# Kernel tuning notes

Measured on AMD Instinct MI355X. Metric: run time of the kernel, lower is better.

Reference implementation:

```python
import jax, jax.numpy as jnp
import numpy as np

NUM_HEADS = 4

def setup_inputs() -> dict:
    key = jax.random.key(0)
    ks = jax.random.split(key, 5)
    B, N, C = 2, 4096, 256
    s = 0.02
    return {
        "x": jax.random.normal(ks[0], (B, N, C), dtype=jnp.float32),
        "qkv_w": jax.random.normal(ks[1], (3 * C, C), dtype=jnp.float32) * s,
        "qkv_b": jax.random.normal(ks[2], (3 * C,), dtype=jnp.float32) * s,
        "out_w": jax.random.normal(ks[3], (C, C), dtype=jnp.float32) * s,
        "out_b": jax.random.normal(ks[4], (C,), dtype=jnp.float32) * s,
    }

def reference(x, qkv_w, qkv_b, out_w, out_b):
    # x: [B, N, C]; manual multi-head self-attention (eval mode, dropout off)
    B, N, C = x.shape
    H = NUM_HEADS
    D = C // H
    qkv = x @ qkv_w.T + qkv_b                      # [B, N, 3C]
    qkv = qkv.reshape(B, N, 3, H, D)
    qkv = jnp.transpose(qkv, (2, 0, 3, 1, 4))      # [3, B, H, N, D]
    q, k, v = qkv[0], qkv[1], qkv[2]
    scale = D ** -0.5
    attn = jnp.einsum('bhnd,bhmd->bhnm', q, k) * scale  # [B, H, N, N]
    attn = jax.nn.softmax(attn, axis=-1)
    out = jnp.einsum('bhnm,bhmd->bhnd', attn, v)   # [B, H, N, D]
    out = jnp.transpose(out, (0, 2, 1, 3)).reshape(B, N, C)
    return out @ out_w.T + out_b
```

## Files before the change

### kernel.cpp

```cpp
#include <hip/hip_runtime.h>

typedef __bf16 bf16x8 __attribute__((ext_vector_type(8)));
typedef float f32x4 __attribute__((ext_vector_type(4)));

#define MFMA_BF16(a, b, c) __builtin_amdgcn_mfma_f32_16x16x32_bf16((a), (b), (c), 0, 0, 0)

#define C1 0.18033688f

static __device__ __forceinline__ unsigned short f2bf(float f) {
    unsigned int u = __float_as_uint(f);
    unsigned int r = (u + 0x7fffu + ((u >> 16) & 1u)) >> 16;
    return (unsigned short)r;
}
static __device__ __forceinline__ float bf2f(unsigned short us) {
    return __uint_as_float(((unsigned int)us) << 16);
}
static __device__ __forceinline__ float exp2_hw(float x) {
    float r;
    asm("v_exp_f32 %0, %1" : "=v"(r) : "v"(x));
    return r;
}
static __device__ __forceinline__ unsigned pack_rh(float a, float b) {
    return __byte_perm(__float_as_uint(a) + 0x8000u, __float_as_uint(b) + 0x8000u, 0x7632);
}
static __device__ __forceinline__ void gload16(const void* g, void* l) {
    __builtin_amdgcn_global_load_lds(
        (const __attribute__((address_space(1))) unsigned int*)g,
        (__attribute__((address_space(3))) unsigned int*)l, 16, 0, 0);
}

static __device__ __forceinline__ void conv_seg8(const void* src, unsigned short* dst, int n,
                                                 int lb, bool f32) {
    const int base = lb * 2048 + (int)threadIdx.x * 8;
    if (base < n) {
        if (f32) {
            const float4 u0 = *(const float4*)((const float*)src + base);
            const float4 u1 = *(const float4*)((const float*)src + base + 4);
            uint4 p;
            p.x = pack_rh(u0.x, u0.y);
            p.y = pack_rh(u0.z, u0.w);
            p.z = pack_rh(u1.x, u1.y);
            p.w = pack_rh(u1.z, u1.w);
            *(uint4*)(dst + base) = p;
        } else {
            *(uint4*)(dst + base) = *(const uint4*)((const unsigned short*)src + base);
        }
    }
}

__global__ __launch_bounds__(256) void convert_kernel(
    const void* __restrict__ x, const void* __restrict__ qw, const void* __restrict__ qb,
    const void* __restrict__ ow, const void* __restrict__ ob,
    unsigned short* __restrict__ xb, unsigned short* __restrict__ qwb,
    unsigned short* __restrict__ qbb, unsigned short* __restrict__ owb,
    unsigned short* __restrict__ obb, int* __restrict__ flag) {
    __shared__ int tot;
    if (threadIdx.x == 0) tot = 0;
    __syncthreads();
    {
        unsigned short v = ((const unsigned short*)x)[threadIdx.x];
        int e = (v >> 7) & 0xFF;
        if (e >= 195) atomicAdd(&tot, 1);
    }
    __syncthreads();
    const bool f32 = (tot >= 8);
    if (blockIdx.x == 0 && threadIdx.x == 0) flag[0] = f32 ? 1 : 0;

    const int bid = blockIdx.x;
    if (bid < 1024)       conv_seg8(x,  xb,  2097152, bid,        f32);
    else if (bid < 1120)  conv_seg8(qw, qwb, 196608,  bid - 1024, f32);
    else if (bid < 1121)  conv_seg8(qb, qbb, 768,     bid - 1120, f32);
    else if (bid < 1153)  conv_seg8(ow, owb, 65536,   bid - 1121, f32);
    else                  conv_seg8(ob, obb, 256,     bid - 1153, f32);
}

template <bool QKV>
__global__ __launch_bounds__(256) void gemm_kernel(
    const unsigned short* __restrict__ A, const unsigned short* __restrict__ W,
    const unsigned short* __restrict__ bias, unsigned short* __restrict__ Cb,
    float* __restrict__ Cf, const int* __restrict__ flag,
    unsigned short* __restrict__ Vt, int Nout) {
    constexpr int K = 256;
    __shared__ __align__(16) char sm[16384];

    const int tid = threadIdx.x;
    const int lane = tid & 63;
    const int wv = tid >> 6;
    const int m16 = lane & 15;
    const int quad = lane >> 4;
    const int bm = blockIdx.x * 64;
    const int bn = blockIdx.y * 64;

    int bgo[2], blo[2];
#pragma unroll
    for (int i = 0; i < 2; i++) {
        const int c = wv * 128 + i * 64 + lane;
        const int r = c >> 3, g = (c & 7) ^ (r & 7);
        bgo[i] = r * (K * 2) + g * 16;
        blo[i] = c * 16;
    }
    int bro[4][2];
#pragma unroll
    for (int t = 0; t < 4; t++)
#pragma unroll
        for (int ks = 0; ks < 2; ks++) {
            const int row = t * 16 + m16;
            bro[t][ks] = row * 64 + ((4 * ks + quad) ^ (m16 & 7)) * 8;
        }

    const char* bg = (const char*)(W + (size_t)bn * K);
    const unsigned short* ap = A + (size_t)(bm + wv * 16 + m16) * K + quad * 8;

#pragma unroll
    for (int i = 0; i < 2; i++) gload16(bg + bgo[i], sm + blo[i]);
    bf16x8 a0 = *(const bf16x8*)(ap);
    bf16x8 a1 = *(const bf16x8*)(ap + 32);

    f32x4 acc[4] = {};
#pragma unroll
    for (int kb = 0; kb < 4; kb++) {
        __syncthreads();
        const int cur = kb & 1;
        bf16x8 a0n, a1n;
        if (kb < 3) {
            bg += 128;
            char* Bdst = sm + (cur ^ 1) * 8192;
#pragma unroll
            for (int i = 0; i < 2; i++) gload16(bg + bgo[i], Bdst + blo[i]);
            a0n = *(const bf16x8*)(ap + (kb + 1) * 64);
            a1n = *(const bf16x8*)(ap + (kb + 1) * 64 + 32);
        }
        const unsigned short* Blds = (const unsigned short*)(sm + cur * 8192);
#pragma unroll
        for (int ks = 0; ks < 2; ks++) {
            const bf16x8 a = ks ? a1 : a0;
#pragma unroll
            for (int t = 0; t < 4; t++) {
                const bf16x8 b = *(const bf16x8*)(Blds + bro[t][ks]);
                acc[t] = MFMA_BF16(a, b, acc[t]);
            }
        }
        if (kb < 3) {
            a0 = a0n;
            a1 = a1n;
        }
    }

    if (QKV && bn >= 512) {
        __syncthreads();
        unsigned short* tr = (unsigned short*)sm;
        const int lr = wv * 16 + quad * 4;
#pragma unroll
        for (int t = 0; t < 4; t++) {
            const float bv = bf2f(bias[bn + t * 16 + m16]);
            uint2 w;
            w.x = pack_rh(acc[t][0] + bv, acc[t][1] + bv);
            w.y = pack_rh(acc[t][2] + bv, acc[t][3] + bv);
            *(uint2*)&tr[(t * 16 + m16) * 72 + lr] = w;
        }
        __syncthreads();
        const int d = tid >> 2;
        const int ch = (tid & 3) * 16;
        const uint4 o4a = *(const uint4*)&tr[d * 72 + ch];
        const uint4 o4b = *(const uint4*)&tr[d * 72 + ch + 8];
        const int hh = (bn - 512) >> 6;
        const int bb = bm >> 12, n0 = bm & 4095;
        unsigned short* vdst = &Vt[((size_t)((bb * 4 + hh) * 64 + d)) * 4096 + n0 + ch];
        *(uint4*)(vdst) = o4a;
        *(uint4*)(vdst + 8) = o4b;
        return;
    }

    const bool outf = (!QKV) && (flag != nullptr) && (*flag != 0);
    const int row0 = bm + wv * 16 + quad * 4;
#pragma unroll
    for (int t = 0; t < 4; t++) {
        const int col = bn + t * 16 + m16;
        const float bv = bf2f(bias[col]);
        float v[4];
#pragma unroll
        for (int r = 0; r < 4; r++) v[r] = acc[t][r] + bv;
        if (QKV) {
            const float sc = (col < 256) ? C1 : 1.0f;
#pragma unroll
            for (int r = 0; r < 4; r++)
                Cb[(size_t)(row0 + r) * 768 + col] = f2bf(v[r] * sc);
        } else {
            if (outf) {
#pragma unroll
                for (int r = 0; r < 4; r++) Cf[(size_t)(row0 + r) * Nout + col] = v[r];
            } else {
#pragma unroll
                for (int r = 0; r < 4; r++) Cb[(size_t)(row0 + r) * Nout + col] = f2bf(v[r]);
            }
        }
    }
}

__global__ __launch_bounds__(256) void attn_kernel(
    const unsigned short* __restrict__ qkv, const unsigned short* __restrict__ Vt,
    unsigned short* __restrict__ attn, int iters) {
    const int N = 4096, C3 = 768;
    __shared__ __align__(16) char sm[65536];

    const int tid = threadIdx.x;
    const int lane = tid & 63;
    const int wv = tid >> 6;
    const int m16 = lane & 15;
    const int quad = lane >> 4;

    const int bh = blockIdx.x & 7;
    const int qt = blockIdx.x >> 3;
    const int b = bh >> 2, h = bh & 3;

    bf16x8 qf[4][2];
#pragma unroll
    for (int j = 0; j < 4; j++)
#pragma unroll
        for (int ks = 0; ks < 2; ks++)
            qf[j][ks] = *(const bf16x8*)(qkv + ((size_t)b * N + qt * 64 + j * 16 + m16) * C3 +
                                         h * 64 + ks * 32 + quad * 8);

    uint4 ones_u;
    ones_u.x = ones_u.y = ones_u.z = ones_u.w = 0x3F803F80u;
    const bf16x8 ones = *(const bf16x8*)&ones_u;

    int kgo[4], vgo[4], klo[4], vlo[4];
#pragma unroll
    for (int i = 0; i < 4; i++) {
        const int c = i * 64 + lane;
        const int r = c >> 3, g = (c & 7) ^ (r & 7);
        kgo[i] = (wv * 32 + r) * 1536 + g * 16;
        klo[i] = c * 16;
        const int d = c >> 2, js = c & 3, jg = js ^ ((d >> 2) & 3);
        vgo[i] = d * 8192 + wv * 64 + jg * 16;
        vlo[i] = c * 16;
    }
    int kro[2][2];
#pragma unroll
    for (int mb = 0; mb < 2; mb++)
#pragma unroll
        for (int ks = 0; ks < 2; ks++) {
            const int row = mb * 16 + m16;
            kro[mb][ks] = row * 64 + ((4 * ks + quad) ^ (m16 & 7)) * 8;
        }
    int vroA[4];
#pragma unroll
    for (int t = 0; t < 4; t++) {
        const int d = t * 16 + m16;
        const int c0 = (quad >> 1) ^ ((d >> 2) & 3);
        vroA[t] = d * 32 + c0 * 8 + (quad & 1) * 4;
    }

    char* Kreg0 = sm + wv * 8192;
    char* Vreg0 = sm + 32768 + wv * 8192;

    const char* kgp = (const char*)(qkv + (size_t)b * N * C3 + 256 + h * 64);
    const char* vgp = (const char*)(Vt + (size_t)bh * 64 * N);

#pragma unroll
    for (int i = 0; i < 4; i++) gload16(kgp + kgo[i], Kreg0 + klo[i]);
#pragma unroll
    for (int i = 0; i < 4; i++) gload16(vgp + vgo[i], Vreg0 + vlo[i]);
    const char* kgn = kgp + 128 * 1536;
    const char* vgn = vgp + 256;

    f32x4 o[4][4] = {};
    f32x4 o1[4] = {};

    for (int kt = 0; kt < iters; ++kt) {
        const int cur = kt & 1;
        if (kt + 1 < iters) {
            char* Kdst = Kreg0 + (cur ^ 1) * 4096;
            char* Vdst = Vreg0 + (cur ^ 1) * 4096;
#pragma unroll
            for (int i = 0; i < 4; i++) gload16(kgn + kgo[i], Kdst + klo[i]);
#pragma unroll
            for (int i = 0; i < 4; i++) gload16(vgn + vgo[i], Vdst + vlo[i]);
            kgn += 128 * 1536;
            vgn += 256;
            asm volatile("s_waitcnt vmcnt(12)" ::: "memory");
        } else {
            asm volatile("s_waitcnt vmcnt(4)" ::: "memory");
        }
        const unsigned short* Kb = (const unsigned short*)(Kreg0 + cur * 4096);
        const unsigned short* Vb = (const unsigned short*)(Vreg0 + cur * 4096);

        f32x4 s[2][4] = {};
        __builtin_amdgcn_s_setprio(1);
#pragma unroll
        for (int mb = 0; mb < 2; mb++)
#pragma unroll
            for (int ks = 0; ks < 2; ks++) {
                const bf16x8 ka = *(const bf16x8*)(Kb + kro[mb][ks]);
#pragma unroll
                for (int j = 0; j < 4; j++) s[mb][j] = MFMA_BF16(ka, qf[j][ks], s[mb][j]);
            }
        __builtin_amdgcn_s_setprio(0);

        bf16x8 pa[4];
#pragma unroll
        for (int j = 0; j < 4; j++) {
            const float e0 = exp2_hw(s[0][j][0]);
            const float e1 = exp2_hw(s[0][j][1]);
            const float e2 = exp2_hw(s[0][j][2]);
            const float e3 = exp2_hw(s[0][j][3]);
            const float e4 = exp2_hw(s[1][j][0]);
            const float e5 = exp2_hw(s[1][j][1]);
            const float e6 = exp2_hw(s[1][j][2]);
            const float e7 = exp2_hw(s[1][j][3]);
            uint4 pw;
            pw.x = pack_rh(e0, e1);
            pw.y = pack_rh(e2, e3);
            pw.z = pack_rh(e4, e5);
            pw.w = pack_rh(e6, e7);
            pa[j] = *(const bf16x8*)&pw;
        }

        if (kt + 1 < iters) {
            asm volatile("s_waitcnt vmcnt(8)" ::: "memory");
        } else {
            asm volatile("s_waitcnt vmcnt(0)" ::: "memory");
        }

        __builtin_amdgcn_s_setprio(1);
#pragma unroll
        for (int j = 0; j < 4; j++) o1[j] = MFMA_BF16(pa[j], ones, o1[j]);
#pragma unroll
        for (int t = 0; t < 4; t++) {
            const uint2 va = *(const uint2*)(Vb + vroA[t]);
            const uint2 vc = *(const uint2*)(Vb + (vroA[t] ^ 16));
            uint4 vv;
            vv.x = va.x;
            vv.y = va.y;
            vv.z = vc.x;
            vv.w = vc.y;
            const bf16x8 vb = *(const bf16x8*)&vv;
#pragma unroll
            for (int j = 0; j < 4; j++) o[j][t] = MFMA_BF16(pa[j], vb, o[j][t]);
        }
        __builtin_amdgcn_s_setprio(0);
    }

    __syncthreads();
    float* Ored = (float*)sm;
    float* lsum = (float*)(sm + 16384);
    if (m16 == 0) {
#pragma unroll
        for (int j = 0; j < 4; j++)
#pragma unroll
            for (int r = 0; r < 4; r++)
                lsum[wv * 64 + j * 16 + quad * 4 + r] = o1[j][r];
    }
    const int row = tid >> 4;
    const int col = (tid & 15) * 4;
#pragma unroll
    for (int j = 0; j < 4; j++) {
#pragma unroll
        for (int t = 0; t < 4; t++)
#pragma unroll
            for (int r = 0; r < 4; r++)
                Ored[(wv * 16 + quad * 4 + r) * 64 + t * 16 + m16] = o[j][t][r];
        __syncthreads();
        f32x4 sum = *(f32x4*)&Ored[row * 64 + col];
        sum += *(f32x4*)&Ored[1024 + row * 64 + col];
        sum += *(f32x4*)&Ored[2048 + row * 64 + col];
        sum += *(f32x4*)&Ored[3072 + row * 64 + col];
        const float lq = lsum[j * 16 + row] + lsum[64 + j * 16 + row] +
                         lsum[128 + j * 16 + row] + lsum[192 + j * 16 + row];
        const int n = qt * 64 + j * 16 + row;
        const float inv = 1.0f / lq;
        uint2 w;
        w.x = pack_rh(sum[0] * inv, sum[1] * inv);
        w.y = pack_rh(sum[2] * inv, sum[3] * inv);
        *(uint2*)&attn[((size_t)b * N + n) * 256 + h * 64 + col] = w;
        __syncthreads();
    }
}

extern "C" void kernel_launch(void* const* d_in, const int* in_sizes, int n_in,
                              void* d_out, int out_size, void* d_ws, size_t ws_size,
                              hipStream_t stream) {
    const int B = 2, N = 4096, H = 4;
    const int M = B * N;

    char* wsb = (char*)d_ws;
    int* flag = (int*)wsb;
    unsigned short* xb      = (unsigned short*)(wsb + 64);
    unsigned short* qwb     = xb + 2097152;
    unsigned short* qbb     = qwb + 196608;
    unsigned short* owb     = qbb + 768;
    unsigned short* obb     = owb + 65536;
    unsigned short* qkv_ws  = obb + 256;
    unsigned short* Vt_ws   = qkv_ws + 6291456;
    unsigned short* attn_ws = Vt_ws + 2097152;

    convert_kernel<<<1154, 256, 0, stream>>>(d_in[0], d_in[1], d_in[2], d_in[3], d_in[4],
                                             xb, qwb, qbb, owb, obb, flag);

    gemm_kernel<true><<<dim3(M / 64, 768 / 64), 256, 0, stream>>>(
        xb, qwb, qbb, qkv_ws, nullptr, nullptr, Vt_ws, 768);

    attn_kernel<<<512, 256, 0, stream>>>(qkv_ws, Vt_ws, attn_ws, 32);

    gemm_kernel<false><<<dim3(M / 64, 256 / 64), 256, 0, stream>>>(
        attn_ws, owb, obb, (unsigned short*)d_out, (float*)d_out, flag, nullptr, 256);
}
```

Before: 136.0 us.

## Split attention KV range across eight waves with half-size K/V slabs per wave

```diff
diff --git a/kernel.cpp b/kernel.cpp
--- a/kernel.cpp
+++ b/kernel.cpp
@@ -197,7 +197,7 @@
     }
 }
 
-__global__ __launch_bounds__(256) void attn_kernel(
+__global__ __launch_bounds__(512, 4) void attn_kernel(
     const unsigned short* __restrict__ qkv, const unsigned short* __restrict__ Vt,
     unsigned short* __restrict__ attn, int iters) {
     const int N = 4096, C3 = 768;
@@ -225,126 +225,143 @@
     ones_u.x = ones_u.y = ones_u.z = ones_u.w = 0x3F803F80u;
     const bf16x8 ones = *(const bf16x8*)&ones_u;
 
-    int kgo[4], vgo[4], klo[4], vlo[4];
-#pragma unroll
-    for (int i = 0; i < 4; i++) {
+    int kgo[2], klo[2], vgo[2], vlo[2];
+#pragma unroll
+    for (int i = 0; i < 2; i++) {
         const int c = i * 64 + lane;
         const int r = c >> 3, g = (c & 7) ^ (r & 7);
-        kgo[i] = (wv * 32 + r) * 1536 + g * 16;
+        kgo[i] = (wv * 16 + r) * 1536 + g * 16;
         klo[i] = c * 16;
-        const int d = c >> 2, js = c & 3, jg = js ^ ((d >> 2) & 3);
-        vgo[i] = d * 8192 + wv * 64 + jg * 16;
+        const int d = c >> 1, js = c & 1, jg = js ^ ((d >> 2) & 1);
+        vgo[i] = d * 8192 + wv * 32 + jg * 16;
         vlo[i] = c * 16;
     }
-    int kro[2][2];
-#pragma unroll
-    for (int mb = 0; mb < 2; mb++)
-#pragma unroll
-        for (int ks = 0; ks < 2; ks++) {
-            const int row = mb * 16 + m16;
-            kro[mb][ks] = row * 64 + ((4 * ks + quad) ^ (m16 & 7)) * 8;
-        }
-    int vroA[4];
+    int kro[2];
+#pragma unroll
+    for (int ks = 0; ks < 2; ks++)
+        kro[ks] = m16 * 64 + ((4 * ks + quad) ^ (m16 & 7)) * 8;
+    int vro[4];
 #pragma unroll
     for (int t = 0; t < 4; t++) {
         const int d = t * 16 + m16;
-        const int c0 = (quad >> 1) ^ ((d >> 2) & 3);
-        vroA[t] = d * 32 + c0 * 8 + (quad & 1) * 4;
-    }
-
-    char* Kreg0 = sm + wv * 8192;
-    char* Vreg0 = sm + 32768 + wv * 8192;
+        vro[t] = d * 16 + (((quad >> 1) ^ ((d >> 2) & 1)) * 8) + (quad & 1) * 4;
+    }
+
+    char* Kslab = sm + wv * 4096;
+    char* Vslab = sm + 32768 + wv * 4096;
 
     const char* kgp = (const char*)(qkv + (size_t)b * N * C3 + 256 + h * 64);
     const char* vgp = (const char*)(Vt + (size_t)bh * 64 * N);
 
 #pragma unroll
-    for (int i = 0; i < 4; i++) gload16(kgp + kgo[i], Kreg0 + klo[i]);
-#pragma unroll
-    for (int i = 0; i < 4; i++) gload16(vgp + vgo[i], Vreg0 + vlo[i]);
+    for (int i = 0; i < 2; i++) gload16(kgp + kgo[i], Kslab + klo[i]);
+#pragma unroll
+    for (int i = 0; i < 2; i++) gload16(vgp + vgo[i], Vslab + vlo[i]);
+#pragma unroll
+    for (int i = 0; i < 2; i++) gload16(vgp + 256 + vgo[i], Vslab + 2048 + vlo[i]);
     const char* kgn = kgp + 128 * 1536;
-    const char* vgn = vgp + 256;
+    const char* vgn = vgp + 512;
 
     f32x4 o[4][4] = {};
     f32x4 o1[4] = {};
 
-    for (int kt = 0; kt < iters; ++kt) {
-        const int cur = kt & 1;
-        if (kt + 1 < iters) {
-            char* Kdst = Kreg0 + (cur ^ 1) * 4096;
-            char* Vdst = Vreg0 + (cur ^ 1) * 4096;
-#pragma unroll
-            for (int i = 0; i < 4; i++) gload16(kgn + kgo[i], Kdst + klo[i]);
-#pragma unroll
-            for (int i = 0; i < 4; i++) gload16(vgn + vgo[i], Vdst + vlo[i]);
+    const int nw = iters >> 1;
+    for (int k2 = 0; k2 < nw; ++k2) {
+#pragma unroll
+        for (int i = 0; i < 2; i++) gload16(kgn + kgo[i], Kslab + 2048 + klo[i]);
+        kgn += 128 * 1536;
+        asm volatile("s_waitcnt vmcnt(6)" ::: "memory");
+        f32x4 sA[4] = {};
+        {
+            const unsigned short* Kb = (const unsigned short*)Kslab;
+            __builtin_amdgcn_s_setprio(1);
+#pragma unroll
+            for (int ks = 0; ks < 2; ks++) {
+                const bf16x8 ka = *(const bf16x8*)(Kb + kro[ks]);
+#pragma unroll
+                for (int j = 0; j < 4; j++) sA[j] = MFMA_BF16(ka, qf[j][ks], sA[j]);
+            }
+            __builtin_amdgcn_s_setprio(0);
+        }
+        uint2 plo[4];
+#pragma unroll
+        for (int j = 0; j < 4; j++) {
+            const float e0 = exp2_hw(sA[j][0]);
+            const float e1 = exp2_hw(sA[j][1]);
+            const float e2 = exp2_hw(sA[j][2]);
+            const float e3 = exp2_hw(sA[j][3]);
+            plo[j].x = pack_rh(e0, e1);
+            plo[j].y = pack_rh(e2, e3);
+        }
+
+        if (k2 + 1 < nw) {
+#pragma unroll
+            for (int i = 0; i < 2; i++) gload16(kgn + kgo[i], Kslab + klo[i]);
             kgn += 128 * 1536;
-            vgn += 256;
-            asm volatile("s_waitcnt vmcnt(12)" ::: "memory");
-        } else {
-            asm volatile("s_waitcnt vmcnt(4)" ::: "memory");
-        }
-        const unsigned short* Kb = (const unsigned short*)(Kreg0 + cur * 4096);
-        const unsigned short* Vb = (const unsigned short*)(Vreg0 + cur * 4096);
-
-        f32x4 s[2][4] = {};
-        __builtin_amdgcn_s_setprio(1);
-#pragma unroll
-        for (int mb = 0; mb < 2; mb++)
-#pragma unroll
-            for (int ks = 0; ks < 2; ks++) {
-                const bf16x8 ka = *(const bf16x8*)(Kb + kro[mb][ks]);
-#pragma unroll
-                for (int j = 0; j < 4; j++) s[mb][j] = MFMA_BF16(ka, qf[j][ks], s[mb][j]);
-            }
-        __builtin_amdgcn_s_setprio(0);
-
-        bf16x8 pa[4];
-#pragma unroll
-        for (int j = 0; j < 4; j++) {
-            const float e0 = exp2_hw(s[0][j][0]);
-            const float e1 = exp2_hw(s[0][j][1]);
-            const float e2 = exp2_hw(s[0][j][2]);
-            const float e3 = exp2_hw(s[0][j][3]);
-            const float e4 = exp2_hw(s[1][j][0]);
-            const float e5 = exp2_hw(s[1][j][1]);
-            const float e6 = exp2_hw(s[1][j][2]);
-            const float e7 = exp2_hw(s[1][j][3]);
-            uint4 pw;
-            pw.x = pack_rh(e0, e1);
-            pw.y = pack_rh(e2, e3);
-            pw.z = pack_rh(e4, e5);
-            pw.w = pack_rh(e6, e7);
-            pa[j] = *(const bf16x8*)&pw;
-        }
-
-        if (kt + 1 < iters) {
-            asm volatile("s_waitcnt vmcnt(8)" ::: "memory");
+            asm volatile("s_waitcnt vmcnt(2)" ::: "memory");
         } else {
             asm volatile("s_waitcnt vmcnt(0)" ::: "memory");
         }
-
-        __builtin_amdgcn_s_setprio(1);
-#pragma unroll
-        for (int j = 0; j < 4; j++) o1[j] = MFMA_BF16(pa[j], ones, o1[j]);
-#pragma unroll
-        for (int t = 0; t < 4; t++) {
-            const uint2 va = *(const uint2*)(Vb + vroA[t]);
-            const uint2 vc = *(const uint2*)(Vb + (vroA[t] ^ 16));
-            uint4 vv;
-            vv.x = va.x;
-            vv.y = va.y;
-            vv.z = vc.x;
-            vv.w = vc.y;
-            const bf16x8 vb = *(const bf16x8*)&vv;
-#pragma unroll
-            for (int j = 0; j < 4; j++) o[j][t] = MFMA_BF16(pa[j], vb, o[j][t]);
-        }
-        __builtin_amdgcn_s_setprio(0);
+        f32x4 sB[4] = {};
+        {
+            const unsigned short* Kb = (const unsigned short*)(Kslab + 2048);
+            __builtin_amdgcn_s_setprio(1);
+#pragma unroll
+            for (int ks = 0; ks < 2; ks++) {
+                const bf16x8 ka = *(const bf16x8*)(Kb + kro[ks]);
+#pragma unroll
+                for (int j = 0; j < 4; j++) sB[j] = MFMA_BF16(ka, qf[j][ks], sB[j]);
+            }
+            __builtin_amdgcn_s_setprio(0);
+        }
+        bf16x8 pa[4];
+#pragma unroll
+        for (int j = 0; j < 4; j++) {
+            const float e0 = exp2_hw(sB[j][0]);
+            const float e1 = exp2_hw(sB[j][1]);
+            const float e2 = exp2_hw(sB[j][2]);
+            const float e3 = exp2_hw(sB[j][3]);
+            uint4 pw;
+            pw.x = plo[j].x;
+            pw.y = plo[j].y;
+            pw.z = pack_rh(e0, e1);
+            pw.w = pack_rh(e2, e3);
+            pa[j] = *(const bf16x8*)&pw;
+        }
+
+        {
+            const unsigned short* Vb = (const unsigned short*)Vslab;
+            __builtin_amdgcn_s_setprio(1);
+#pragma unroll
+            for (int j = 0; j < 4; j++) o1[j] = MFMA_BF16(pa[j], ones, o1[j]);
+#pragma unroll
+            for (int t = 0; t < 4; t++) {
+                const uint2 va = *(const uint2*)(Vb + vro[t]);
+                const uint2 vc = *(const uint2*)(Vb + 1024 + vro[t]);
+                uint4 vv;
+                vv.x = va.x;
+                vv.y = va.y;
+                vv.z = vc.x;
+                vv.w = vc.y;
+                const bf16x8 vb = *(const bf16x8*)&vv;
+#pragma unroll
+                for (int j = 0; j < 4; j++) o[j][t] = MFMA_BF16(pa[j], vb, o[j][t]);
+            }
+            __builtin_amdgcn_s_setprio(0);
+        }
+        if (k2 + 1 < nw) {
+            __builtin_amdgcn_sched_barrier(0);
+#pragma unroll
+            for (int i = 0; i < 2; i++) gload16(vgn + vgo[i], Vslab + vlo[i]);
+#pragma unroll
+            for (int i = 0; i < 2; i++) gload16(vgn + 256 + vgo[i], Vslab + 2048 + vlo[i]);
+            vgn += 512;
+        }
     }
 
     __syncthreads();
     float* Ored = (float*)sm;
-    float* lsum = (float*)(sm + 16384);
+    float* lsum = (float*)(sm + 32768);
     if (m16 == 0) {
 #pragma unroll
         for (int j = 0; j < 4; j++)
@@ -352,28 +369,28 @@
             for (int r = 0; r < 4; r++)
                 lsum[wv * 64 + j * 16 + quad * 4 + r] = o1[j][r];
     }
-    const int row = tid >> 4;
-    const int col = (tid & 15) * 4;
+    const int q16 = tid >> 5;
+    const int dp = (tid & 31) * 2;
 #pragma unroll
     for (int j = 0; j < 4; j++) {
 #pragma unroll
         for (int t = 0; t < 4; t++)
 #pragma unroll
             for (int r = 0; r < 4; r++)
-                Ored[(wv * 16 + quad * 4 + r) * 64 + t * 16 + m16] = o[j][t][r];
+                Ored[wv * 1024 + (quad * 4 + r) * 64 + t * 16 + m16] = o[j][t][r];
         __syncthreads();
-        f32x4 sum = *(f32x4*)&Ored[row * 64 + col];
-        sum += *(f32x4*)&Ored[1024 + row * 64 + col];
-        sum += *(f32x4*)&Ored[2048 + row * 64 + col];
-        sum += *(f32x4*)&Ored[3072 + row * 64 + col];
-        const float lq = lsum[j * 16 + row] + lsum[64 + j * 16 + row] +
-                         lsum[128 + j * 16 + row] + lsum[192 + j * 16 + row];
-        const int n = qt * 64 + j * 16 + row;
+        float s0 = 0.f, s1 = 0.f, lq = 0.f;
+#pragma unroll
+        for (int w = 0; w < 8; w++) {
+            const float* src = &Ored[w * 1024 + q16 * 64 + dp];
+            s0 += src[0];
+            s1 += src[1];
+            lq += lsum[w * 64 + j * 16 + q16];
+        }
         const float inv = 1.0f / lq;
-        uint2 w;
-        w.x = pack_rh(sum[0] * inv, sum[1] * inv);
-        w.y = pack_rh(sum[2] * inv, sum[3] * inv);
-        *(uint2*)&attn[((size_t)b * N + n) * 256 + h * 64 + col] = w;
+        const int n = qt * 64 + j * 16 + q16;
+        *(unsigned*)&attn[((size_t)b * N + n) * 256 + h * 64 + dp] =
+            pack_rh(s0 * inv, s1 * inv);
         __syncthreads();
     }
 }
@@ -401,7 +418,7 @@
     gemm_kernel<true><<<dim3(M / 64, 768 / 64), 256, 0, stream>>>(
         xb, qwb, qbb, qkv_ws, nullptr, nullptr, Vt_ws, 768);
 
-    attn_kernel<<<512, 256, 0, stream>>>(qkv_ws, Vt_ws, attn_ws, 32);
+    attn_kernel<<<512, 512, 0, stream>>>(qkv_ws, Vt_ws, attn_ws, 32);
 
     gemm_kernel<false><<<dim3(M / 64, 256 / 64), 256, 0, stream>>>(
         attn_ws, owb, obb, (unsigned short*)d_out, (float*)d_out, flag, nullptr, 256);
```

Measured after the change: 288.7 us. 2.12x slower.
